# Kernel optimization log

Hardware: AMD Instinct MI355X
Metric: run time of the kernel (lower is better)

The kernel has to match this reference:

```python
import jax, jax.numpy as jnp
import numpy as np

N = 100000   # nodes
E = 3200000  # edges
G = 512      # graphs in batch
EPS = 1e-5   # batchnorm eps


def _lin(key, fan_in, fan_out):
    return jax.random.normal(key, (fan_in, fan_out), jnp.float32) / np.sqrt(fan_in)


def setup_inputs() -> dict:
    key = jax.random.key(0)
    ks = jax.random.split(key, 12)
    x = jax.random.normal(ks[0], (N, 2), jnp.float32)
    edge_index = jax.random.randint(ks[1], (2, E), 0, N, dtype=jnp.int64)
    batch_index = jnp.sort(jax.random.randint(ks[2], (N,), 0, G, dtype=jnp.int64))
    w = (8, 32, 128)
    return {
        "x": x, "edge_index": edge_index, "batch_index": batch_index,
        "W1": _lin(ks[3], 2, w[0]),   "b1": jnp.zeros((w[0],), jnp.float32),
        "g1": jnp.ones((w[0],), jnp.float32),  "be1": jnp.zeros((w[0],), jnp.float32),
        "W2": _lin(ks[4], w[0], w[1]), "b2": jnp.zeros((w[1],), jnp.float32),
        "g2": jnp.ones((w[1],), jnp.float32),  "be2": jnp.zeros((w[1],), jnp.float32),
        "W3": _lin(ks[5], w[1], w[2]), "b3": jnp.zeros((w[2],), jnp.float32),
        "g3": jnp.ones((w[2],), jnp.float32),  "be3": jnp.zeros((w[2],), jnp.float32),
        "Wl": _lin(ks[6], w[2], 3),    "bl": jnp.zeros((3,), jnp.float32),
    }


def _gcn_norm(edge_index):
    # add self loops, symmetric normalization (PyG GCNConv default)
    loops = jnp.arange(N, dtype=edge_index.dtype)
    src = jnp.concatenate([edge_index[0], loops])
    dst = jnp.concatenate([edge_index[1], loops])
    deg = jax.ops.segment_sum(jnp.ones_like(dst, jnp.float32), dst, num_segments=N)
    dis = jnp.where(deg > 0, jax.lax.rsqrt(jnp.maximum(deg, 1.0)), 0.0)
    norm = dis[src] * dis[dst]  # [E+N]
    return src, dst, norm


def _gcn_conv(h, W, b, src, dst, norm):
    h = h @ W                                   # [N, out]
    msg = h[src] * norm[:, None]                # gather + scale
    return jax.ops.segment_sum(msg, dst, num_segments=N) + b


def _bn(h, g, b):
    # training-mode batchnorm over node dim
    m = jnp.mean(h, axis=0)
    v = jnp.mean(jnp.square(h - m), axis=0)
    return (h - m) * jax.lax.rsqrt(v + EPS) * g + b


def reference(x, edge_index, batch_index, W1, b1, g1, be1, W2, b2, g2, be2,
              W3, b3, g3, be3, Wl, bl):
    src, dst, norm = _gcn_norm(edge_index)
    h = _bn(jax.nn.relu(_gcn_conv(x, W1, b1, src, dst, norm)), g1, be1)
    h = _bn(jax.nn.relu(_gcn_conv(h, W2, b2, src, dst, norm)), g2, be2)
    h = _bn(jax.nn.relu(_gcn_conv(h, W3, b3, src, dst, norm)), g3, be3)
    pooled = jax.ops.segment_max(h, batch_index, num_segments=G)  # [G, 128]
    logits = pooled @ Wl + bl                                     # [G, 3]
    return jax.nn.log_softmax(logits, axis=1)
```

## Files before the change

### kernel.cpp

```cpp
#include <hip/hip_runtime.h>
#include <hip/hip_bf16.h>
#include <hip/hip_fp16.h>
#include <math.h>

#define N_NODES 100000
#define N_EDGES 3200000
#define N_GRAPHS 512
#define BN_EPS 1e-5f
#define NBIN ((N_NODES + 511) / 512)
#define CHUNK 8192
#define NCHUNK ((N_EDGES + CHUNK - 1) / CHUNK)
#define STORE_CAP (N_EDGES + 16 * NBIN * NCHUNK)
#define LSEG 98
#define NSEGB ((N_NODES + LSEG - 1) / LSEG)
#define NSTATB ((N_NODES + 127) / 128)

typedef _Float16 half8_t __attribute__((ext_vector_type(8)));
typedef float float4_t __attribute__((ext_vector_type(4)));

struct alignas(8) h4 { __half2 a, b; };
struct alignas(16) h8s { __half2 h[4]; };


__global__ void k_hist2(const int* __restrict__ dst, int* __restrict__ hists) {
    __shared__ int h[NBIN];
    for (int i = threadIdx.x; i < NBIN; i += blockDim.x) h[i] = 0;
    __syncthreads();
    int e0 = blockIdx.x * CHUNK;
    int e1 = min(e0 + CHUNK, N_EDGES);
    for (int e = e0 + threadIdx.x; e < e1; e += blockDim.x)
        atomicAdd(&h[dst[e] >> 9], 1);
    __syncthreads();
    for (int i = threadIdx.x; i < NBIN; i += blockDim.x)
        hists[i * NCHUNK + blockIdx.x] = h[i];
}

__global__ void k_scan2(int* __restrict__ hists, int* __restrict__ ghist) {
    int b = blockIdx.x;
    int lane = threadIdx.x;
    int carry = 0;
    int base = b * NCHUNK;
    for (int c0 = 0; c0 < NCHUNK; c0 += 64) {
        int c = c0 + lane;
        int v = (c < NCHUNK) ? hists[base + c] : 0;
        int pv = (v + 15) & ~15;
        int inc = pv;
#pragma unroll
        for (int off = 1; off < 64; off <<= 1) {
            int u = __shfl_up(inc, off, 64);
            if (lane >= off) inc += u;
        }
        if (c < NCHUNK) hists[base + c] = inc - pv + carry;
        carry += __shfl(inc, 63, 64);
    }
    if (lane == 0) ghist[b] = carry;
}

__global__ void k_binscan(const int* __restrict__ ghist, int* __restrict__ bbase) {
    __shared__ int sd[512];
    int t = threadIdx.x;
    int v = (t < NBIN) ? ghist[t] : 0;
    sd[t] = v;
    __syncthreads();
    for (int off = 1; off < 512; off <<= 1) {
        int u = (t >= off) ? sd[t - off] : 0;
        __syncthreads();
        sd[t] += u;
        __syncthreads();
    }
    if (t < NBIN) bbase[t] = sd[t] - v;
    if (t == 511) bbase[NBIN] = sd[511];
}

__global__ void k_scatter(const int* __restrict__ src, const int* __restrict__ dst,
                          const int* __restrict__ bbase, const int* __restrict__ hists,
                          int* __restrict__ store) {
    __shared__ int cur[NBIN];
    for (int i = threadIdx.x; i < NBIN; i += blockDim.x)
        cur[i] = bbase[i] + hists[i * NCHUNK + blockIdx.x];
    __syncthreads();
    int e0 = blockIdx.x * CHUNK;
    int e1 = min(e0 + CHUNK, N_EDGES);
    for (int e = e0 + threadIdx.x; e < e1; e += blockDim.x) {
        int d = dst[e];
        int b = d >> 9;
        int pos = atomicAdd(&cur[b], 1);
        store[pos] = (src[e] << 9) | (d & 511);
    }
    __syncthreads();
    for (int i = threadIdx.x; i < NBIN; i += blockDim.x) {
        int p = cur[i];
        int end = (p + 15) & ~15;
        for (; p < end; ++p) store[p] = -1;
    }
}

__global__ void k_csr_build(const int* __restrict__ bbase, const int* __restrict__ store,
                            const float* __restrict__ x, int* __restrict__ offs,
                            int* __restrict__ ends, float* __restrict__ dis,
                            float* __restrict__ rdis, float4* __restrict__ xd,
                            int* __restrict__ csr) {
    __shared__ int cnt[512], cur[512], wsum[4];
    int b = blockIdx.x;
    int n0 = b << 9;
    int e0 = bbase[b], e1 = bbase[b + 1];
    int t = threadIdx.x;
    int lane = t & 63, wid = t >> 6;
    if (t < 512) cnt[t] = 0;
    __syncthreads();
    for (int e = e0 + t; e < e1; e += 1024) {
        int p = store[e];
        if (p >= 0) atomicAdd(&cnt[p & 511], 1);
    }
    __syncthreads();
    int c0 = 0, c1 = 0, pair = 0, inc = 0;
    if (t < 256) {
        c0 = cnt[2 * t];
        c1 = cnt[2 * t + 1];
        pair = c0 + c1;
        inc = pair;
#pragma unroll
        for (int off = 1; off < 64; off <<= 1) {
            int u = __shfl_up(inc, off, 64);
            if (lane >= off) inc += u;
        }
        if (lane == 63) wsum[wid] = inc;
    }
    __syncthreads();
    if (t < 256) {
        int wo = 0;
        for (int w = 0; w < wid; ++w) wo += wsum[w];
        int ex = inc - pair + wo;
        cur[2 * t] = ex;
        cur[2 * t + 1] = ex + c0;
#pragma unroll
        for (int j = 0; j < 2; ++j) {
            int n = n0 + 2 * t + j;
            int cc = j ? c1 : c0;
            int exx = j ? ex + c0 : ex;
            if (n < N_NODES) {
                offs[n] = e0 + exx;
                ends[n] = e0 + exx + cc;
                float dn = rsqrtf(1.0f + (float)cc);
                dis[n] = dn;
                rdis[n] = sqrtf(1.0f + (float)cc);
                float2 xv = *(const float2*)(x + 2 * (size_t)n);
                xd[n] = make_float4(dn * xv.x, dn * xv.y, dn, 0.f);
            } else if (n == N_NODES) {
                xd[N_NODES] = make_float4(0.f, 0.f, 0.f, 0.f);
            }
        }
    }
    __syncthreads();
    for (int e = e0 + t; e < e1; e += 1024) {
        int p = store[e];
        if (p >= 0) {
            int pos = e0 + atomicAdd(&cur[p & 511], 1);
            csr[pos] = p >> 9;
        }
    }
}


__global__ void k_agg1(const float4* __restrict__ xd, const int* __restrict__ offs,
                       const int* __restrict__ ends, const int* __restrict__ csr,
                       const float* __restrict__ W1, const float* __restrict__ b1,
                       float* __restrict__ svec, __half* __restrict__ ys1) {
    __shared__ float sW[16], sb[8];
    int t = threadIdx.x;
    if (t < 16) sW[t] = W1[t];
    if (t < 8) sb[t] = b1[t];
    __syncthreads();
    int wave = t >> 6, lane = t & 63;
    int nsub = lane >> 4, eg = lane & 15;
    int node = ((blockIdx.x * 4 + wave) << 2) + nsub;
    int e0 = offs[node], e1 = ends[node];
    float ax = 0.f, ay = 0.f, as = 0.f;
    for (int e = e0 + eg; e < e1; e += 32) {
        int s0 = csr[e];
        int s1 = (e + 16 < e1) ? csr[e + 16] : N_NODES;
        float4 v0 = xd[s0];
        float4 v1 = xd[s1];
        ax += v0.x + v1.x;
        ay += v0.y + v1.y;
        as += v0.z + v1.z;
    }
#pragma unroll
    for (int off = 1; off < 16; off <<= 1) {
        ax += __shfl_xor(ax, off, 64);
        ay += __shfl_xor(ay, off, 64);
        as += __shfl_xor(as, off, 64);
    }
    if (eg == 0) {
        float4 xn = xd[node];
        float dn = xn.z;
        float u0x = dn * (ax + xn.x);
        float u0y = dn * (ay + xn.y);
        svec[node] = dn * (as + xn.z);
        float y[8];
#pragma unroll
        for (int f = 0; f < 8; ++f)
            y[f] = dn * fmaxf(u0x * sW[f] + u0y * sW[8 + f] + sb[f], 0.f);
        h8s o;
#pragma unroll
        for (int q = 0; q < 4; ++q) o.h[q] = __floats2half2_rn(y[2 * q], y[2 * q + 1]);
        *(h8s*)(ys1 + (size_t)node * 8) = o;
    }
}


__global__ void k_prep2(const float* __restrict__ stats, const float* __restrict__ gamma,
                        const float* __restrict__ beta, const float* __restrict__ W2,
                        float* __restrict__ W2p, float* __restrict__ cw2,
                        __half* __restrict__ ys1) {
    __shared__ float a1[8], c1[8];
    int t = threadIdx.x;
    if (t < 8) {
        float inv_n = 1.0f / (float)N_NODES;
        float m = stats[t] * inv_n;
        float v = stats[8 + t] * inv_n - m * m;
        float a = gamma[t] * rsqrtf(v + BN_EPS);
        a1[t] = a;
        c1[t] = beta[t] - m * a;
    }
    __syncthreads();
    W2p[t] = a1[t >> 5] * W2[t];
    if (t < 32) {
        float cb = 0.f;
#pragma unroll
        for (int i = 0; i < 8; ++i) cb += c1[i] * W2[i * 32 + t];
        cw2[t] = cb;
    }
    if (t == 128) *(int4*)(ys1 + (size_t)N_NODES * 8) = make_int4(0, 0, 0, 0);
}


__global__ void k_agg2(const __half* __restrict__ ys1, const int* __restrict__ offs,
                       const int* __restrict__ ends, const int* __restrict__ csr,
                       const float* __restrict__ dis, const float* __restrict__ svec,
                       const float* __restrict__ W2p, const float* __restrict__ cw2,
                       const float* __restrict__ b2, __half* __restrict__ ys2) {
    __shared__ float sW[256], sC[32], sB[32];
    int t = threadIdx.x;
    sW[t] = W2p[t];
    if (t < 32) { sC[t] = cw2[t]; sB[t] = b2[t]; }
    __syncthreads();
    int wave = t >> 6, lane = t & 63;
    int nsub = lane >> 3, eg = (lane >> 1) & 3, chunk = lane & 1;
    int node = ((blockIdx.x * 4 + wave) << 3) + nsub;
    int e0 = offs[node], e1 = ends[node];
    float a0 = 0.f, a1 = 0.f, a2 = 0.f, a3 = 0.f;
    const __half* hp = ys1 + chunk * 4;
    for (int e = e0 + eg; e < e1; e += 8) {
        int s0 = csr[e];
        int s1 = (e + 4 < e1) ? csr[e + 4] : N_NODES;
        h4 v0 = *(const h4*)(hp + (size_t)s0 * 8);
        h4 v1 = *(const h4*)(hp + (size_t)s1 * 8);
        a0 += __low2float(v0.a) + __low2float(v1.a);
        a1 += __high2float(v0.a) + __high2float(v1.a);
        a2 += __low2float(v0.b) + __low2float(v1.b);
        a3 += __high2float(v0.b) + __high2float(v1.b);
    }
    if (eg == 0) {
        h4 v = *(const h4*)(hp + (size_t)node * 8);
        a0 += __low2float(v.a);
        a1 += __high2float(v.a);
        a2 += __low2float(v.b);
        a3 += __high2float(v.b);
    }
#pragma unroll
    for (int off = 2; off < 8; off <<= 1) {
        a0 += __shfl_xor(a0, off, 64);
        a1 += __shfl_xor(a1, off, 64);
        a2 += __shfl_xor(a2, off, 64);
        a3 += __shfl_xor(a3, off, 64);
    }
    int lb = nsub << 3;
    float u[8];
    u[0] = __shfl(a0, lb, 64);     u[1] = __shfl(a1, lb, 64);
    u[2] = __shfl(a2, lb, 64);     u[3] = __shfl(a3, lb, 64);
    u[4] = __shfl(a0, lb + 1, 64); u[5] = __shfl(a1, lb + 1, 64);
    u[6] = __shfl(a2, lb + 1, 64); u[7] = __shfl(a3, lb + 1, 64);
    float dn = dis[node];
    float sv = svec[node];
#pragma unroll
    for (int i = 0; i < 8; ++i) u[i] *= dn;
    int c0 = (lane & 7) * 4;
    float y[4];
#pragma unroll
    for (int k = 0; k < 4; ++k) {
        int col = c0 + k;
        float conv = sB[col] + sv * sC[col];
#pragma unroll
        for (int i = 0; i < 8; ++i) conv += u[i] * sW[i * 32 + col];
        y[k] = dn * fmaxf(conv, 0.f);
    }
    h4 o;
    o.a = __floats2half2_rn(y[0], y[1]);
    o.b = __floats2half2_rn(y[2], y[3]);
    *(h4*)(ys2 + (size_t)node * 32 + c0) = o;
}


__global__ void k_prep3(const float* __restrict__ stats, const float* __restrict__ gamma,
                        const float* __restrict__ beta, const float* __restrict__ W3,
                        __half* __restrict__ wfrag, float* __restrict__ cw3,
                        __half* __restrict__ ys2) {
    __shared__ float a2[32], c2[32];
    int t = threadIdx.x;
    if (t < 32) {
        float inv_n = 1.0f / (float)N_NODES;
        float m = stats[t] * inv_n;
        float v = stats[32 + t] * inv_n - m * m;
        float a = gamma[t] * rsqrtf(v + BN_EPS);
        a2[t] = a;
        c2[t] = beta[t] - m * a;
    }
    __syncthreads();
    {
        int g = t >> 6, kq = (t >> 4) & 3, c = t & 15;
#pragma unroll
        for (int j = 0; j < 8; ++j) {
            int k = kq * 8 + j;
            wfrag[(size_t)t * 8 + j] = __float2half(a2[k] * W3[k * 128 + g * 16 + c]);
        }
    }
    if (t < 128) {
        float cb = 0.f;
#pragma unroll
        for (int k = 0; k < 32; ++k) cb += c2[k] * W3[k * 128 + t];
        cw3[t] = cb;
    }
    if (t >= 480 && t < 496)
        ((__half2*)(ys2 + (size_t)N_NODES * 32))[t - 480] =
            __half2{__float2half(0.f), __float2half(0.f)};
}


__global__ void k_agg3(const __half* __restrict__ ys2, const int* __restrict__ offs,
                       const int* __restrict__ ends, const int* __restrict__ csr,
                       const float* __restrict__ dis, __half* __restrict__ u2) {
    int wave = threadIdx.x >> 6;
    int lane = threadIdx.x & 63;
    int node = blockIdx.x * 4 + wave;
    if (node >= N_NODES) return;
    int chunk = lane & 7;
    int eg = lane >> 3;
    int e0 = offs[node], e1 = ends[node];
    float ax = 0.f, ay = 0.f, az = 0.f, aw = 0.f;
    const __half* hp = ys2 + (size_t)chunk * 4;
    for (int e = e0 + eg; e < e1; e += 32) {
        int s0 = csr[e];
        int s1 = (e + 8 < e1) ? csr[e + 8] : N_NODES;
        int s2 = (e + 16 < e1) ? csr[e + 16] : N_NODES;
        int s3 = (e + 24 < e1) ? csr[e + 24] : N_NODES;
        h4 v0 = *(const h4*)(hp + (size_t)s0 * 32);
        h4 v1 = *(const h4*)(hp + (size_t)s1 * 32);
        h4 v2 = *(const h4*)(hp + (size_t)s2 * 32);
        h4 v3 = *(const h4*)(hp + (size_t)s3 * 32);
        ax += __low2float(v0.a) + __low2float(v1.a) + __low2float(v2.a) + __low2float(v3.a);
        ay += __high2float(v0.a) + __high2float(v1.a) + __high2float(v2.a) + __high2float(v3.a);
        az += __low2float(v0.b) + __low2float(v1.b) + __low2float(v2.b) + __low2float(v3.b);
        aw += __high2float(v0.b) + __high2float(v1.b) + __high2float(v2.b) + __high2float(v3.b);
    }
    if (eg == 0) {
        h4 v = *(const h4*)(hp + (size_t)node * 32);
        ax += __low2float(v.a);
        ay += __high2float(v.a);
        az += __low2float(v.b);
        aw += __high2float(v.b);
    }
#pragma unroll
    for (int off = 8; off < 64; off <<= 1) {
        ax += __shfl_xor(ax, off, 64);
        ay += __shfl_xor(ay, off, 64);
        az += __shfl_xor(az, off, 64);
        aw += __shfl_xor(aw, off, 64);
    }
    if (lane < 8) {
        float dn = dis[node];
        h4 o;
        o.a = __floats2half2_rn(dn * ax, dn * ay);
        o.b = __floats2half2_rn(dn * az, dn * aw);
        *(h4*)(u2 + (size_t)node * 32 + chunk * 4) = o;
    }
}


__global__ void k_mm_mfma(const __half* __restrict__ u2, const __half* __restrict__ wfrag,
                          const float* __restrict__ cw3, const float* __restrict__ b3,
                          const float* __restrict__ svec, const float* __restrict__ dis,
                          __half* __restrict__ ys3) {
    int wave = threadIdx.x >> 6;
    int lane = threadIdx.x & 63;
    int n0 = (blockIdx.x * 4 + wave) * 16;
    if (n0 >= N_NODES) return;
    int m = lane & 15;
    int kq = lane >> 4;

    half8_t af = *(const half8_t*)(u2 + (size_t)(n0 + m) * 32 + kq * 8);

    float4_t accs[8];
#pragma unroll
    for (int g = 0; g < 8; ++g) {
        float4_t acc = {0.f, 0.f, 0.f, 0.f};
        half8_t bf = *(const half8_t*)(wfrag + (size_t)((g * 4 + kq) * 16 + m) * 8);
        accs[g] = __builtin_amdgcn_mfma_f32_16x16x32_f16(af, bf, acc, 0, 0, 0);
    }
    float sv[4], dn[4];
#pragma unroll
    for (int r = 0; r < 4; ++r) {
        sv[r] = svec[n0 + kq * 4 + r];
        dn[r] = dis[n0 + kq * 4 + r];
    }
#pragma unroll
    for (int g = 0; g < 8; ++g) {
        float cwf = cw3[g * 16 + m];
        float bf3 = b3[g * 16 + m];
#pragma unroll
        for (int r = 0; r < 4; ++r) {
            float y = fmaxf(accs[g][r] + sv[r] * cwf + bf3, 0.f);
            ys3[(size_t)(n0 + kq * 4 + r) * 128 + g * 16 + m] = __float2half(dn[r] * y);
        }
    }
}


template <int FOUT>
__global__ void k_stats(const __half* __restrict__ ys, const float* __restrict__ rdis,
                        float* __restrict__ stats) {
    constexpr int GP = 256 / FOUT;
    int f = threadIdx.x % FOUT, g = threadIdx.x / FOUT;
    float s = 0.f, s2 = 0.f;
    for (int n = blockIdx.x * GP + g; n < N_NODES; n += gridDim.x * GP) {
        float v = __half2float(ys[(size_t)n * FOUT + f]) * rdis[n];
        s += v;
        s2 += v * v;
    }
    __shared__ float ls[256], ls2[256];
    ls[threadIdx.x] = s;
    ls2[threadIdx.x] = s2;
    __syncthreads();
    if (g == 0) {
        for (int gg = 1; gg < GP; ++gg) {
            s += ls[gg * FOUT + f];
            s2 += ls2[gg * FOUT + f];
        }
        atomicAdd(&stats[f], s);
        atomicAdd(&stats[FOUT + f], s2);
    }
}


__global__ void k_stats128(const __half* __restrict__ ys, const float* __restrict__ rdis,
                           float* __restrict__ part) {
    int t = threadIdx.x;
    int chunk = t & 15, row = t >> 4;
    int n0 = blockIdx.x * 128;
    float s[8] = {0, 0, 0, 0, 0, 0, 0, 0};
    float s2[8] = {0, 0, 0, 0, 0, 0, 0, 0};
#pragma unroll
    for (int i = 0; i < 8; ++i) {
        int n = n0 + i * 16 + row;
        if (n < N_NODES) {
            float r = rdis[n];
            h8s v = *(const h8s*)(ys + (size_t)n * 128 + chunk * 8);
#pragma unroll
            for (int q = 0; q < 4; ++q) {
                float v0 = __low2float(v.h[q]) * r;
                float v1 = __high2float(v.h[q]) * r;
                s[2 * q] += v0;  s2[2 * q] += v0 * v0;
                s[2 * q + 1] += v1;  s2[2 * q + 1] += v1 * v1;
            }
        }
    }
#pragma unroll
    for (int off = 16; off < 64; off <<= 1)
#pragma unroll
        for (int j = 0; j < 8; ++j) {
            s[j] += __shfl_xor(s[j], off, 64);
            s2[j] += __shfl_xor(s2[j], off, 64);
        }
    __shared__ float sm[256];
    sm[t] = 0.f;
    __syncthreads();
    if ((t & 63) < 16) {
#pragma unroll
        for (int j = 0; j < 8; ++j) {
            atomicAdd(&sm[chunk * 8 + j], s[j]);
            atomicAdd(&sm[128 + chunk * 8 + j], s2[j]);
        }
    }
    __syncthreads();
    part[(size_t)blockIdx.x * 256 + t] = sm[t];
}

__global__ void k_stats_red(const float* __restrict__ part, float* __restrict__ stats) {
    int i = blockIdx.x;
    int t = threadIdx.x;
    float s = 0.f;
    for (int b = t; b < NSTATB; b += 256) s += part[(size_t)b * 256 + i];
    __shared__ float sm[256];
    sm[t] = s;
    __syncthreads();
    for (int st = 128; st > 0; st >>= 1) {
        if (t < st) sm[t] += sm[t + st];
        __syncthreads();
    }
    if (t == 0) stats[i] = sm[0];
}


__global__ void k_pool1(const __half* __restrict__ ys3, const float* __restrict__ rdis,
                        const int* __restrict__ batch, int* __restrict__ gmax,
                        int* __restrict__ gmin) {
    __shared__ int sb[LSEG];
    __shared__ float sr[LSEG];
    int n0 = blockIdx.x * LSEG;
    int n1 = min(n0 + LSEG, N_NODES);
    int L = n1 - n0;
    int f = threadIdx.x;
    for (int i = f; i < L; i += 128) { sb[i] = batch[n0 + i]; sr[i] = rdis[n0 + i]; }
    __syncthreads();
    if (L <= 0) return;
    int cg = sb[0];
    int mx = 0;
    int mn = 0x7F800000;
    for (int i = 0; i < L; ++i) {
        int g = sb[i];
        if (g != cg) {
            atomicMax(&gmax[cg * 128 + f], mx);
            atomicMin(&gmin[cg * 128 + f], mn);
            cg = g; mx = 0; mn = 0x7F800000;
        }
        float v = __half2float(ys3[(size_t)(n0 + i) * 128 + f]) * sr[i];
        int b = __float_as_int(v);
        mx = max(mx, b);
        mn = min(mn, b);
    }
    atomicMax(&gmax[cg * 128 + f], mx);
    atomicMin(&gmin[cg * 128 + f], mn);
}


__device__ __forceinline__ int lower_bound_dev(const int* __restrict__ a, int val) {
    int lo = 0, hi = N_NODES;
    while (lo < hi) {
        int mid = (lo + hi) >> 1;
        if (a[mid] < val) lo = mid + 1; else hi = mid;
    }
    return lo;
}

__global__ void k_poolhead(const int* __restrict__ gmax, const int* __restrict__ gmin,
                           const int* __restrict__ batch, const float* __restrict__ stats,
                           const float* __restrict__ gamma, const float* __restrict__ beta,
                           const float* __restrict__ Wl, const float* __restrict__ bl,
                           float* __restrict__ out) {
    int g = blockIdx.x;
    int f = threadIdx.x;
    float inv_n = 1.0f / (float)N_NODES;
    float m = stats[f] * inv_n;
    float var = stats[128 + f] * inv_n - m * m;
    float a = gamma[f] * rsqrtf(var + BN_EPS);
    float c = beta[f] - m * a;
    int s = lower_bound_dev(batch, g);
    int e = lower_bound_dev(batch, g + 1);
    float mx = __int_as_float(gmax[g * 128 + f]);
    float mn = __int_as_float(gmin[g * 128 + f]);
    float r;
    if (e > s) r = (a >= 0.f) ? (a * mx + c) : (a * mn + c);
    else r = -INFINITY;
    __shared__ float l[3][128];
    l[0][f] = r * Wl[f * 3 + 0];
    l[1][f] = r * Wl[f * 3 + 1];
    l[2][f] = r * Wl[f * 3 + 2];
    __syncthreads();
    for (int st = 64; st > 0; st >>= 1) {
        if (f < st) {
            l[0][f] += l[0][f + st];
            l[1][f] += l[1][f + st];
            l[2][f] += l[2][f + st];
        }
        __syncthreads();
    }
    if (f == 0) {
        float l0 = l[0][0] + bl[0], l1 = l[1][0] + bl[1], l2 = l[2][0] + bl[2];
        float mxl = fmaxf(l0, fmaxf(l1, l2));
        float lse = mxl + logf(expf(l0 - mxl) + expf(l1 - mxl) + expf(l2 - mxl));
        out[g * 3 + 0] = l0 - lse;
        out[g * 3 + 1] = l1 - lse;
        out[g * 3 + 2] = l2 - lse;
    }
}


extern "C" void kernel_launch(void* const* d_in, const int* in_sizes, int n_in,
                              void* d_out, int out_size, void* d_ws, size_t ws_size,
                              hipStream_t stream) {
    const float* x   = (const float*)d_in[0];
    const int* ei    = (const int*)d_in[1];
    const int* src   = ei;
    const int* dst   = ei + N_EDGES;
    const int* batch = (const int*)d_in[2];
    const float *W1 = (const float*)d_in[3],  *b1 = (const float*)d_in[4];
    const float *g1 = (const float*)d_in[5],  *be1 = (const float*)d_in[6];
    const float *W2 = (const float*)d_in[7],  *b2 = (const float*)d_in[8];
    const float *g2 = (const float*)d_in[9],  *be2 = (const float*)d_in[10];
    const float *W3 = (const float*)d_in[11], *b3 = (const float*)d_in[12];
    const float *g3 = (const float*)d_in[13], *be3 = (const float*)d_in[14];
    const float *Wl = (const float*)d_in[15], *bl = (const float*)d_in[16];
    float* out = (float*)d_out;

    int* base = (int*)d_ws;
    size_t o = 0;
    float* stats1 = (float*)(base + o); o += 256;
    float* stats2 = (float*)(base + o); o += 256;
    float* stats3 = (float*)(base + o); o += 256;
    int* gmax     = base + o; o += (size_t)N_GRAPHS * 128;
    size_t zero_words = o;
    int* gmin     = base + o; o += (size_t)N_GRAPHS * 128;
    int* bbase    = base + o; o += NBIN + 4;
    int* ghist    = base + o; o += NBIN + 4;
    int* hists    = base + o; o += ((size_t)NBIN * NCHUNK + 3) & ~3ULL;
    float* W2p    = (float*)(base + o); o += 256;
    float* cw2    = (float*)(base + o); o += 32;
    __half* wfrag = (__half*)(base + o); o += 2048;
    float* cw3    = (float*)(base + o); o += 128;
    int* offs     = base + o; o += 100000;
    int* ends     = base + o; o += 100000;
    int* store    = base + o; o += STORE_CAP;
    int* csr      = base + o; o += STORE_CAP;
    float* dis    = (float*)(base + o); o += N_NODES;
    float* rdis   = (float*)(base + o); o += N_NODES;
    float* svec   = (float*)(base + o); o += N_NODES;
    float* spart  = (float*)(base + o); o += (size_t)NSTATB * 256;
    float4* xd    = (float4*)(base + o); o += (size_t)(N_NODES + 1) * 4;
    __half* ys1   = (__half*)(base + o); o += (size_t)(N_NODES + 1) * 4;
    __half* ys2   = (__half*)(base + o); o += (size_t)(N_NODES + 1) * 16;
    __half* u2    = (__half*)(base + o); o += (size_t)N_NODES * 16;
    __half* ys3   = (__half*)(base + o); o += (size_t)N_NODES * 64;
    if (ws_size < o * 4) return;

    const int TB = 256;

    hipMemsetAsync(base, 0, zero_words * 4, stream);
    hipMemsetAsync(gmin, 0x7F, (size_t)N_GRAPHS * 128 * 4, stream);

    k_hist2<<<NCHUNK, TB, 0, stream>>>(dst, hists);
    k_scan2<<<NBIN, 64, 0, stream>>>(hists, ghist);
    k_binscan<<<1, 512, 0, stream>>>(ghist, bbase);
    k_scatter<<<NCHUNK, TB, 0, stream>>>(src, dst, bbase, hists, store);
    k_csr_build<<<NBIN, 1024, 0, stream>>>(bbase, store, x, offs, ends, dis, rdis, xd, csr);

    k_agg1<<<N_NODES / 16, TB, 0, stream>>>(xd, offs, ends, csr, W1, b1, svec, ys1);
    k_stats<8><<<256, 256, 0, stream>>>(ys1, rdis, stats1);
    k_prep2<<<1, 256, 0, stream>>>(stats1, g1, be1, W2, W2p, cw2, ys1);

    k_agg2<<<N_NODES / 32, TB, 0, stream>>>(ys1, offs, ends, csr, dis, svec, W2p, cw2, b2, ys2);
    k_stats<32><<<256, 256, 0, stream>>>(ys2, rdis, stats2);
    k_prep3<<<1, 512, 0, stream>>>(stats2, g2, be2, W3, wfrag, cw3, ys2);

    k_agg3<<<(N_NODES + 3) / 4, TB, 0, stream>>>(ys2, offs, ends, csr, dis, u2);
    k_mm_mfma<<<(N_NODES + 63) / 64, 256, 0, stream>>>(u2, wfrag, cw3, b3, svec, dis, ys3);
    k_stats128<<<NSTATB, 256, 0, stream>>>(ys3, rdis, spart);
    k_stats_red<<<256, 256, 0, stream>>>(spart, stats3);

    k_pool1<<<NSEGB, 128, 0, stream>>>(ys3, rdis, batch, gmax, gmin);
    k_poolhead<<<N_GRAPHS, 128, 0, stream>>>(gmax, gmin, batch, stats3, g3, be3, Wl, bl, out);
}
```

Measured before the change: 380.5 us.

## Split layer-3 aggregation into two passes by source-node half for cache locality

The CSR build now partitions each node's neighbor list into sources below and above node 50000 and records a mid offset. Layer-3 aggregation is split into two kernels, each gathering from only one half of ys2, so each pass's gather footprint (about 3.2MB of fp16 rows) is more likely to stay resident in L2. The first pass writes an fp16 partial sum that the second pass reads back and adds. This costs an extra launch, an extra intermediate buffer round-trip, a second read of the CSR offsets, and one more fp16 rounding step.

```diff
diff --git a/kernel.cpp b/kernel.cpp
--- a/kernel.cpp
+++ b/kernel.cpp
@@ -7,6 +7,7 @@
 #define N_EDGES 3200000
 #define N_GRAPHS 512
 #define BN_EPS 1e-5f
+#define HALF_SRC 50000
 #define NBIN ((N_NODES + 511) / 512)
 #define CHUNK 8192
 #define NCHUNK ((N_EDGES + CHUNK - 1) / CHUNK)
@@ -97,27 +98,30 @@
 
 __global__ void k_csr_build(const int* __restrict__ bbase, const int* __restrict__ store,
                             const float* __restrict__ x, int* __restrict__ offs,
-                            int* __restrict__ ends, float* __restrict__ dis,
-                            float* __restrict__ rdis, float4* __restrict__ xd,
-                            int* __restrict__ csr) {
-    __shared__ int cnt[512], cur[512], wsum[4];
+                            int* __restrict__ mids, int* __restrict__ ends,
+                            float* __restrict__ dis, float* __restrict__ rdis,
+                            float4* __restrict__ xd, int* __restrict__ csr) {
+    __shared__ int cntA[512], cntB[512], curA[512], curB[512], wsum[4];
     int b = blockIdx.x;
     int n0 = b << 9;
     int e0 = bbase[b], e1 = bbase[b + 1];
     int t = threadIdx.x;
     int lane = t & 63, wid = t >> 6;
-    if (t < 512) cnt[t] = 0;
+    if (t < 512) { cntA[t] = 0; cntB[t] = 0; }
     __syncthreads();
     for (int e = e0 + t; e < e1; e += 1024) {
         int p = store[e];
-        if (p >= 0) atomicAdd(&cnt[p & 511], 1);
-    }
-    __syncthreads();
-    int c0 = 0, c1 = 0, pair = 0, inc = 0;
+        if (p >= 0) {
+            int* c = ((p >> 9) < HALF_SRC) ? cntA : cntB;
+            atomicAdd(&c[p & 511], 1);
+        }
+    }
+    __syncthreads();
+    int a0 = 0, b0 = 0, a1 = 0, b1 = 0, pair = 0, inc = 0;
     if (t < 256) {
-        c0 = cnt[2 * t];
-        c1 = cnt[2 * t + 1];
-        pair = c0 + c1;
+        a0 = cntA[2 * t]; b0 = cntB[2 * t];
+        a1 = cntA[2 * t + 1]; b1 = cntB[2 * t + 1];
+        pair = a0 + b0 + a1 + b1;
         inc = pair;
 #pragma unroll
         for (int off = 1; off < 64; off <<= 1) {
@@ -131,15 +135,20 @@
         int wo = 0;
         for (int w = 0; w < wid; ++w) wo += wsum[w];
         int ex = inc - pair + wo;
-        cur[2 * t] = ex;
-        cur[2 * t + 1] = ex + c0;
+        int c0 = a0 + b0, c1 = a1 + b1;
+        curA[2 * t] = ex;
+        curB[2 * t] = ex + a0;
+        curA[2 * t + 1] = ex + c0;
+        curB[2 * t + 1] = ex + c0 + a1;
 #pragma unroll
         for (int j = 0; j < 2; ++j) {
             int n = n0 + 2 * t + j;
+            int aa = j ? a1 : a0;
             int cc = j ? c1 : c0;
             int exx = j ? ex + c0 : ex;
             if (n < N_NODES) {
                 offs[n] = e0 + exx;
+                mids[n] = e0 + exx + aa;
                 ends[n] = e0 + exx + cc;
                 float dn = rsqrtf(1.0f + (float)cc);
                 dis[n] = dn;
@@ -155,8 +164,10 @@
     for (int e = e0 + t; e < e1; e += 1024) {
         int p = store[e];
         if (p >= 0) {
-            int pos = e0 + atomicAdd(&cur[p & 511], 1);
-            csr[pos] = p >> 9;
+            int s = p >> 9;
+            int* c = (s < HALF_SRC) ? curA : curB;
+            int pos = e0 + atomicAdd(&c[p & 511], 1);
+            csr[pos] = s;
         }
     }
 }
@@ -337,16 +348,16 @@
 }
 
 
-__global__ void k_agg3(const __half* __restrict__ ys2, const int* __restrict__ offs,
-                       const int* __restrict__ ends, const int* __restrict__ csr,
-                       const float* __restrict__ dis, __half* __restrict__ u2) {
+__global__ void k_agg3a(const __half* __restrict__ ys2, const int* __restrict__ offs,
+                        const int* __restrict__ mids, const int* __restrict__ csr,
+                        __half* __restrict__ u2p) {
     int wave = threadIdx.x >> 6;
     int lane = threadIdx.x & 63;
     int node = blockIdx.x * 4 + wave;
     if (node >= N_NODES) return;
     int chunk = lane & 7;
     int eg = lane >> 3;
-    int e0 = offs[node], e1 = ends[node];
+    int e0 = offs[node], e1 = mids[node];
     float ax = 0.f, ay = 0.f, az = 0.f, aw = 0.f;
     const __half* hp = ys2 + (size_t)chunk * 4;
     for (int e = e0 + eg; e < e1; e += 32) {
@@ -363,6 +374,49 @@
         az += __low2float(v0.b) + __low2float(v1.b) + __low2float(v2.b) + __low2float(v3.b);
         aw += __high2float(v0.b) + __high2float(v1.b) + __high2float(v2.b) + __high2float(v3.b);
     }
+#pragma unroll
+    for (int off = 8; off < 64; off <<= 1) {
+        ax += __shfl_xor(ax, off, 64);
+        ay += __shfl_xor(ay, off, 64);
+        az += __shfl_xor(az, off, 64);
+        aw += __shfl_xor(aw, off, 64);
+    }
+    if (lane < 8) {
+        h4 o;
+        o.a = __floats2half2_rn(ax, ay);
+        o.b = __floats2half2_rn(az, aw);
+        *(h4*)(u2p + (size_t)node * 32 + chunk * 4) = o;
+    }
+}
+
+
+__global__ void k_agg3b(const __half* __restrict__ ys2, const int* __restrict__ mids,
+                        const int* __restrict__ ends, const int* __restrict__ csr,
+                        const float* __restrict__ dis, const __half* __restrict__ u2p,
+                        __half* __restrict__ u2) {
+    int wave = threadIdx.x >> 6;
+    int lane = threadIdx.x & 63;
+    int node = blockIdx.x * 4 + wave;
+    if (node >= N_NODES) return;
+    int chunk = lane & 7;
+    int eg = lane >> 3;
+    int e0 = mids[node], e1 = ends[node];
+    float ax = 0.f, ay = 0.f, az = 0.f, aw = 0.f;
+    const __half* hp = ys2 + (size_t)chunk * 4;
+    for (int e = e0 + eg; e < e1; e += 32) {
+        int s0 = csr[e];
+        int s1 = (e + 8 < e1) ? csr[e + 8] : N_NODES;
+        int s2 = (e + 16 < e1) ? csr[e + 16] : N_NODES;
+        int s3 = (e + 24 < e1) ? csr[e + 24] : N_NODES;
+        h4 v0 = *(const h4*)(hp + (size_t)s0 * 32);
+        h4 v1 = *(const h4*)(hp + (size_t)s1 * 32);
+        h4 v2 = *(const h4*)(hp + (size_t)s2 * 32);
+        h4 v3 = *(const h4*)(hp + (size_t)s3 * 32);
+        ax += __low2float(v0.a) + __low2float(v1.a) + __low2float(v2.a) + __low2float(v3.a);
+        ay += __high2float(v0.a) + __high2float(v1.a) + __high2float(v2.a) + __high2float(v3.a);
+        az += __low2float(v0.b) + __low2float(v1.b) + __low2float(v2.b) + __low2float(v3.b);
+        aw += __high2float(v0.b) + __high2float(v1.b) + __high2float(v2.b) + __high2float(v3.b);
+    }
     if (eg == 0) {
         h4 v = *(const h4*)(hp + (size_t)node * 32);
         ax += __low2float(v.a);
@@ -378,6 +432,11 @@
         aw += __shfl_xor(aw, off, 64);
     }
     if (lane < 8) {
+        h4 p = *(const h4*)(u2p + (size_t)node * 32 + chunk * 4);
+        ax += __low2float(p.a);
+        ay += __high2float(p.a);
+        az += __low2float(p.b);
+        aw += __high2float(p.b);
         float dn = dis[node];
         h4 o;
         o.a = __floats2half2_rn(dn * ax, dn * ay);
@@ -628,6 +687,7 @@
     __half* wfrag = (__half*)(base + o); o += 2048;
     float* cw3    = (float*)(base + o); o += 128;
     int* offs     = base + o; o += 100000;
+    int* mids     = base + o; o += 100000;
     int* ends     = base + o; o += 100000;
     int* store    = base + o; o += STORE_CAP;
     int* csr      = base + o; o += STORE_CAP;
@@ -638,6 +698,7 @@
     float4* xd    = (float4*)(base + o); o += (size_t)(N_NODES + 1) * 4;
     __half* ys1   = (__half*)(base + o); o += (size_t)(N_NODES + 1) * 4;
     __half* ys2   = (__half*)(base + o); o += (size_t)(N_NODES + 1) * 16;
+    __half* u2p   = (__half*)(base + o); o += (size_t)N_NODES * 16;
     __half* u2    = (__half*)(base + o); o += (size_t)N_NODES * 16;
     __half* ys3   = (__half*)(base + o); o += (size_t)N_NODES * 64;
     if (ws_size < o * 4) return;
@@ -651,7 +712,7 @@
     k_scan2<<<NBIN, 64, 0, stream>>>(hists, ghist);
     k_binscan<<<1, 512, 0, stream>>>(ghist, bbase);
     k_scatter<<<NCHUNK, TB, 0, stream>>>(src, dst, bbase, hists, store);
-    k_csr_build<<<NBIN, 1024, 0, stream>>>(bbase, store, x, offs, ends, dis, rdis, xd, csr);
+    k_csr_build<<<NBIN, 1024, 0, stream>>>(bbase, store, x, offs, mids, ends, dis, rdis, xd, csr);
 
     k_agg1<<<N_NODES / 16, TB, 0, stream>>>(xd, offs, ends, csr, W1, b1, svec, ys1);
     k_stats<8><<<256, 256, 0, stream>>>(ys1, rdis, stats1);
@@ -661,7 +722,8 @@
     k_stats<32><<<256, 256, 0, stream>>>(ys2, rdis, stats2);
     k_prep3<<<1, 512, 0, stream>>>(stats2, g2, be2, W3, wfrag, cw3, ys2);
 
-    k_agg3<<<(N_NODES + 3) / 4, TB, 0, stream>>>(ys2, offs, ends, csr, dis, u2);
+    k_agg3a<<<(N_NODES + 3) / 4, TB, 0, stream>>>(ys2, offs, mids, csr, u2p);
+    k_agg3b<<<(N_NODES + 3) / 4, TB, 0, stream>>>(ys2, mids, ends, csr, dis, u2p, u2);
     k_mm_mfma<<<(N_NODES + 63) / 64, 256, 0, stream>>>(u2, wfrag, cw3, b3, svec, dis, ys3);
     k_stats128<<<NSTATB, 256, 0, stream>>>(ys3, rdis, spart);
     k_stats_red<<<256, 256, 0, stream>>>(spart, stats3);
```

Measured after the change: 387.9 us. No clear change (+1.9%).
